# Kernel optimization log

Measured on AMD Instinct MI355X. Metric: run time of the kernel, lower is better.

## Reference

```python
import jax, jax.numpy as jnp
import numpy as np

D_MODEL = 512
NUM_HEADS = 8
D_K = D_MODEL // NUM_HEADS  # 64
LN_EPS = 1e-5


def setup_inputs() -> dict:
    key = jax.random.key(0)
    ks = jax.random.split(key, 6)
    B, S, D = 8, 1024, D_MODEL
    scale = 1.0 / np.sqrt(D)
    return {
        "query": jax.random.normal(ks[0], (B, S, D), jnp.float32),
        "key": jax.random.normal(ks[1], (B, S, D), jnp.float32),
        "value": jax.random.normal(ks[2], (B, S, D), jnp.float32),
        "Wq": jax.random.normal(ks[3], (D, D), jnp.float32) * scale,
        "bq": jnp.zeros((D,), jnp.float32),
        "Wk": jax.random.normal(ks[4], (D, D), jnp.float32) * scale,
        "bk": jnp.zeros((D,), jnp.float32),
        "Wo": jax.random.normal(ks[5], (D, D * NUM_HEADS), jnp.float32) * (1.0 / np.sqrt(D * NUM_HEADS)),
        "bo": jnp.zeros((D,), jnp.float32),
        "gamma": jnp.ones((D,), jnp.float32),
        "beta": jnp.zeros((D,), jnp.float32),
    }


def reference(query, key, value, Wq, bq, Wk, bk, Wo, bo, gamma, beta):
    B, S, D = value.shape
    h, dk = NUM_HEADS, D_K
    # QK projections -> [B, h, S, dk]
    q = (query @ Wq.T + bq).reshape(B, S, h, dk).transpose(0, 2, 1, 3)
    k = (key @ Wk.T + bk).reshape(B, S, h, dk).transpose(0, 2, 1, 3)
    # scaled dot-product scores [B, h, Sq, Sk]
    scores = jnp.einsum("bhqd,bhkd->bhqk", q, k) / jnp.sqrt(jnp.asarray(dk, q.dtype))
    attn = jax.nn.softmax(scores, axis=-1)
    # value broadcast across heads: value is [B, Sk, D] -> per-head output [B, h, Sq, D]
    x = jnp.einsum("bhqk,bkd->bhqd", attn, value)
    # concat heads -> [B, Sq, h*D], output projection back to D
    x = x.transpose(0, 2, 1, 3).reshape(B, S, h * D)
    x = x @ Wo.T + bo
    # residual + LayerNorm (dropout = identity in eval)
    y = value + x
    mu = jnp.mean(y, axis=-1, keepdims=True)
    var = jnp.var(y, axis=-1, keepdims=True)
    out = (y - mu) * jax.lax.rsqrt(var + LN_EPS) * gamma + beta
    return out, attn
```

## Files before the change

### kernel.cpp

```cpp
#include <hip/hip_runtime.h>
#include <hip/hip_bf16.h>

#define B_ 8
#define S_ 1024
#define D_ 512
#define H_ 8
#define DK_ 64
#define HD_ 4096

typedef __attribute__((ext_vector_type(8))) short bf16x8;
typedef __attribute__((ext_vector_type(4))) float f32x4;

static __device__ __forceinline__ unsigned short f2bf(float f) {
    unsigned u = __float_as_uint(f);
    unsigned r = (u + 0x7fffu + ((u >> 16) & 1u)) >> 16;
    return (unsigned short)r;
}

static __device__ __forceinline__ void gload16(const unsigned short* g, unsigned short* l) {
    __builtin_amdgcn_global_load_lds(
        (const __attribute__((address_space(1))) void*)g,
        (__attribute__((address_space(3))) void*)l, 16, 0, 0);
}

static __device__ __forceinline__ int plidx(int ql, int k) {
    return ql * 1024 + ((((k >> 3) ^ (ql & 7))) << 3) + (k & 7);
}

__global__ __launch_bounds__(256) void prep_kernel(
    const float* __restrict__ query, unsigned short* __restrict__ Xq,
    const float* __restrict__ key,   unsigned short* __restrict__ Xk,
    const float* __restrict__ Wq,    unsigned short* __restrict__ Wqbf,
    const float* __restrict__ Wk,    unsigned short* __restrict__ Wkbf,
    const float* __restrict__ Wo,    unsigned short* __restrict__ Wobf,
    const float* __restrict__ V,     unsigned short* __restrict__ Vt)
{
    __shared__ float tile[32][33];
    const int bid = blockIdx.x;
    const int t = threadIdx.x;
    if (bid < 10752) {
        const float* s; unsigned short* d; int lb;
        if      (bid < 4096) { s = query; d = Xq;   lb = bid; }
        else if (bid < 8192) { s = key;   d = Xk;   lb = bid - 4096; }
        else if (bid < 8448) { s = Wq;    d = Wqbf; lb = bid - 8192; }
        else if (bid < 8704) { s = Wk;    d = Wkbf; lb = bid - 8448; }
        else                 { s = Wo;    d = Wobf; lb = bid - 8704; }
        const size_t i = ((size_t)lb * 256 + t) * 4;
        float4 v = *(const float4*)&s[i];
        ushort4 u = { f2bf(v.x), f2bf(v.y), f2bf(v.z), f2bf(v.w) };
        *(ushort4*)&d[i] = u;
    } else {
        const int idx = bid - 10752;
        const int s0 = (idx & 31) * 32;
        const int e0 = ((idx >> 5) & 15) * 32;
        const int b  = idx >> 9;
        const int r = t >> 3, c4 = (t & 7) * 4;
        float4 v = *(const float4*)&V[((size_t)b * S_ + s0 + r) * D_ + e0 + c4];
        tile[r][c4 + 0] = v.x; tile[r][c4 + 1] = v.y;
        tile[r][c4 + 2] = v.z; tile[r][c4 + 3] = v.w;
        __syncthreads();
        ushort4 u;
        u.x = f2bf(tile[c4 + 0][r]); u.y = f2bf(tile[c4 + 1][r]);
        u.z = f2bf(tile[c4 + 2][r]); u.w = f2bf(tile[c4 + 3][r]);
        *(ushort4*)&Vt[((size_t)b * D_ + e0 + r) * S_ + s0 + c4] = u;
    }
}

template<int KDIM, int MT, int TN, int MODE>
static __device__ __forceinline__ void gemm_body(
    const unsigned short* __restrict__ A, const unsigned short* __restrict__ Bw,
    const float* __restrict__ bias, const float* __restrict__ Vres,
    void* __restrict__ Out, float scale, int nb)
{
    constexpr int NB = 512 / TN;
    constexpr int CF = TN / 32;
    constexpr int MR = MT / 32;
    const int m0 = (nb / NB) * MT;
    const int n0 = (nb % NB) * TN;

    __shared__ __align__(16) unsigned short As[2][MT * 32];
    __shared__ __align__(16) unsigned short Bs[2][TN * 32];

    const int t = threadIdx.x;
    const int wave = t >> 6, lane = t & 63;
    const int wr = wave >> 1, wc = wave & 1;
    const int lr = lane & 15, g = lane >> 4;
    const int gx = (g ^ (lr & 3)) << 3;

    f32x4 acc[MR][CF];
    #pragma unroll
    for (int r = 0; r < MR; ++r)
        #pragma unroll
        for (int c = 0; c < CF; ++c) acc[r][c] = (f32x4){0.f, 0.f, 0.f, 0.f};

    const int sub = lane >> 2;
    const int cb  = (((lane & 3) ^ (sub & 3)) << 3);

    auto stage = [&](int buf, int k0) {
        #pragma unroll
        for (int s = 0; s < MT / 64; ++s) {
            const int chunk = s * 4 + wave;
            const int row = chunk * 16 + sub;
            if constexpr (MODE == 0) {
                gload16(&A[(size_t)(m0 + row) * KDIM + k0 + cb], &As[buf][chunk * 512]);
            } else {
                const int m = m0 + row;
                const int bb = m >> 10, ss = m & 1023;
                const int h = k0 >> 9;
                gload16(&A[(((size_t)(bb * H_ + h)) * S_ + ss) * D_ + (k0 & 511) + cb],
                        &As[buf][chunk * 512]);
            }
        }
        #pragma unroll
        for (int s = 0; s < TN / 64; ++s) {
            const int chunk = s * 4 + wave;
            const int row = chunk * 16 + sub;
            gload16(&Bw[(size_t)(n0 + row) * KDIM + k0 + cb], &Bs[buf][chunk * 512]);
        }
    };
    auto compute = [&](int cur) {
        bf16x8 af[MR], bfr[CF];
        #pragma unroll
        for (int r = 0; r < MR; ++r)
            af[r] = *(const bf16x8*)&As[cur][(wr * (MT / 2) + r * 16 + lr) * 32 + gx];
        #pragma unroll
        for (int c = 0; c < CF; ++c)
            bfr[c] = *(const bf16x8*)&Bs[cur][(wc * (TN / 2) + c * 16 + lr) * 32 + gx];
        __builtin_amdgcn_s_setprio(1);
        #pragma unroll
        for (int c = 0; c < CF; ++c)
            #pragma unroll
            for (int r = 0; r < MR; ++r)
                acc[r][c] = __builtin_amdgcn_mfma_f32_16x16x32_bf16(af[r], bfr[c], acc[r][c], 0, 0, 0);
        __builtin_amdgcn_s_setprio(0);
    };

    const int NT = KDIM / 32;
    stage(0, 0);
    __syncthreads();
    int cur = 0;
    for (int tt = 0; tt < NT - 1; ++tt) {
        stage(cur ^ 1, (tt + 1) * 32);
        compute(cur);
        __syncthreads();
        cur ^= 1;
    }
    compute(cur);

    float bn[CF];
    #pragma unroll
    for (int c = 0; c < CF; ++c) bn[c] = bias[n0 + wc * (TN / 2) + c * 16 + lr];

    #pragma unroll
    for (int r = 0; r < MR; ++r) {
        #pragma unroll
        for (int c = 0; c < CF; ++c) {
            const int n = n0 + wc * (TN / 2) + c * 16 + lr;
            #pragma unroll
            for (int i = 0; i < 4; ++i) {
                const int m = m0 + wr * (MT / 2) + r * 16 + g * 4 + i;
                if constexpr (MODE == 0) {
                    const int srow = m & 1023, bb = m >> 10;
                    const int h = n >> 6, dk = n & 63;
                    ((unsigned short*)Out)[(((size_t)(bb * H_ + h)) * S_ + srow) * DK_ + dk] =
                        f2bf((acc[r][c][i] + bn[c]) * scale);
                } else {
                    const size_t oo = (size_t)m * D_ + n;
                    ((float*)Out)[oo] = acc[r][c][i] + bn[c] + Vres[oo];
                }
            }
        }
    }
}

__global__ __launch_bounds__(256) void proj2_kernel(
    const unsigned short* __restrict__ Xq, const unsigned short* __restrict__ Wqbf,
    const float* __restrict__ bq, unsigned short* __restrict__ Qbf,
    const unsigned short* __restrict__ Xk, const unsigned short* __restrict__ Wkbf,
    const float* __restrict__ bk, unsigned short* __restrict__ Kbf)
{
    const int o = blockIdx.x;
    const bool isQ = o < 512;
    const int ol = isQ ? o : o - 512;
    const int nb = (ol % 8) * 64 + ol / 8;
    gemm_body<512, 128, 64, 0>(isQ ? Xq : Xk, isQ ? Wqbf : Wkbf,
                               isQ ? bq : bk, nullptr,
                               (void*)(isQ ? Qbf : Kbf), isQ ? 0.125f : 1.0f, nb);
}

__global__ __launch_bounds__(256) void out_gemm(
    const unsigned short* __restrict__ AV, const unsigned short* __restrict__ Wobf,
    const float* __restrict__ bo, const float* __restrict__ Vres,
    float* __restrict__ Y)
{
    const int o = blockIdx.x;
    const int nb = (o % 8) * 64 + o / 8;
    gemm_body<4096, 64, 128, 1>(AV, Wobf, bo, Vres, (void*)Y, 0.f, nb);
}

__global__ __launch_bounds__(1024, 4) void fused_attn(
    const unsigned short* __restrict__ Qbf,
    const unsigned short* __restrict__ Kbf,
    const unsigned short* __restrict__ Vt,
    float* __restrict__ attn,
    unsigned short* __restrict__ AV)
{
    const int o = blockIdx.x;
    const int nb = (o & 7) * 128 + (o >> 3);
    const int bh = nb >> 4;
    const int q0 = (nb & 15) * 64;
    const int b = bh >> 3;
    const unsigned short* Qb = Qbf + (size_t)bh * S_ * DK_;
    const unsigned short* Kb = Kbf + (size_t)bh * S_ * DK_;
    const unsigned short* Vb = Vt + (size_t)b * D_ * S_;
    float* outp = attn + ((size_t)bh << 20);

    __shared__ unsigned short PL[64 * 1024];
    __shared__ float redm[64][16];
    __shared__ float rowm[64];

    const int t = threadIdx.x;
    const int wave = t >> 6, lane = t & 63;
    const int wcol = wave * 64;
    const int lr = lane & 15;
    const int g  = lane >> 4;

    f32x4 acc[4][4];
    #pragma unroll
    for (int r = 0; r < 4; ++r)
        #pragma unroll
        for (int c = 0; c < 4; ++c) acc[r][c] = (f32x4){0.f, 0.f, 0.f, 0.f};

    #pragma unroll
    for (int kk = 0; kk < 2; ++kk) {
        bf16x8 af[4];
        #pragma unroll
        for (int r = 0; r < 4; ++r)
            af[r] = *(const bf16x8*)&Kb[(size_t)(wcol + r * 16 + lr) * DK_ + kk * 32 + g * 8];
        bf16x8 qf[4];
        #pragma unroll
        for (int c = 0; c < 4; ++c)
            qf[c] = *(const bf16x8*)&Qb[(size_t)(q0 + c * 16 + lr) * DK_ + kk * 32 + g * 8];
        __builtin_amdgcn_s_setprio(1);
        #pragma unroll
        for (int r = 0; r < 4; ++r)
            #pragma unroll
            for (int c = 0; c < 4; ++c)
                acc[r][c] = __builtin_amdgcn_mfma_f32_16x16x32_bf16(af[r], qf[c], acc[r][c], 0, 0, 0);
        __builtin_amdgcn_s_setprio(0);
    }

    float sloc[4];
    #pragma unroll
    for (int c = 0; c < 4; ++c) {
        float s = 0.f;
        #pragma unroll
        for (int r = 0; r < 4; ++r)
            #pragma unroll
            for (int i = 0; i < 4; ++i) {
                float p = __expf(acc[r][c][i]);
                acc[r][c][i] = p;
                s += p;
            }
        s += __shfl_xor(s, 16);
        s += __shfl_xor(s, 32);
        sloc[c] = s;
    }
    if (lane < 16) {
        #pragma unroll
        for (int c = 0; c < 4; ++c) redm[c * 16 + lane][wave] = sloc[c];
    }
    __syncthreads();
    if (t < 64) {
        float s = redm[t][0];
        #pragma unroll
        for (int w = 1; w < 16; ++w) s += redm[t][w];
        rowm[t] = 1.0f / s;
    }
    __syncthreads();

    #pragma unroll
    for (int c = 0; c < 4; ++c) {
        const int ql = c * 16 + lr;
        const float ri = rowm[ql];
        float* rowp = outp + ((size_t)(q0 + ql) << 10);
        #pragma unroll
        for (int r = 0; r < 4; ++r) {
            f32x4 v = acc[r][c];
            v[0] *= ri; v[1] *= ri; v[2] *= ri; v[3] *= ri;
            const int k = wcol + r * 16 + g * 4;
            *(f32x4*)&rowp[k] = v;
            unsigned p01, p23;
            asm("v_cvt_pk_bf16_f32 %0, %1, %2" : "=v"(p01) : "v"(v[0]), "v"(v[1]));
            asm("v_cvt_pk_bf16_f32 %0, %1, %2" : "=v"(p23) : "v"(v[2]), "v"(v[3]));
            uint2 pk = { p01, p23 };
            *(uint2*)&PL[plidx(ql, k)] = pk;
        }
    }
    __syncthreads();

    const int we = wave * 32;
    f32x4 accv[4][2];
    #pragma unroll
    for (int r = 0; r < 4; ++r)
        #pragma unroll
        for (int c = 0; c < 2; ++c) accv[r][c] = (f32x4){0.f, 0.f, 0.f, 0.f};

    const unsigned short* vp0 = Vb + (size_t)(we + lr) * S_ + g * 8;
    const unsigned short* vp1 = Vb + (size_t)(we + 16 + lr) * S_ + g * 8;
    bf16x8 vf0 = *(const bf16x8*)vp0;
    bf16x8 vf1 = *(const bf16x8*)vp1;

    for (int k0 = 0; k0 < S_; k0 += 32) {
        const int kn = k0 + 32;
        bf16x8 nv0, nv1;
        if (kn < S_) {
            nv0 = *(const bf16x8*)(vp0 + kn);
            nv1 = *(const bf16x8*)(vp1 + kn);
        }
        bf16x8 pa[4];
        #pragma unroll
        for (int r = 0; r < 4; ++r)
            pa[r] = *(const bf16x8*)&PL[plidx(r * 16 + lr, k0 + g * 8)];
        __builtin_amdgcn_s_setprio(1);
        #pragma unroll
        for (int r = 0; r < 4; ++r)
            accv[r][0] = __builtin_amdgcn_mfma_f32_16x16x32_bf16(pa[r], vf0, accv[r][0], 0, 0, 0);
        #pragma unroll
        for (int r = 0; r < 4; ++r)
            accv[r][1] = __builtin_amdgcn_mfma_f32_16x16x32_bf16(pa[r], vf1, accv[r][1], 0, 0, 0);
        __builtin_amdgcn_s_setprio(0);
        if (kn < S_) { vf0 = nv0; vf1 = nv1; }
    }

    #pragma unroll
    for (int r = 0; r < 4; ++r) {
        #pragma unroll
        for (int c = 0; c < 2; ++c) {
            const int e = we + c * 16 + lr;
            #pragma unroll
            for (int i = 0; i < 4; ++i) {
                const int row = q0 + r * 16 + g * 4 + i;
                AV[((size_t)bh * S_ + row) * D_ + e] = f2bf(accv[r][c][i]);
            }
        }
    }
}

__global__ __launch_bounds__(256) void ln_kernel(
    float* __restrict__ Y, const float* __restrict__ gamma,
    const float* __restrict__ beta)
{
    const int lane = threadIdx.x & 63;
    const int wave = threadIdx.x >> 6;
    const size_t row = (size_t)blockIdx.x * 4 + wave;
    float* p = Y + row * D_;
    float4 v0 = *(float4*)&p[lane * 4];
    float4 v1 = *(float4*)&p[256 + lane * 4];
    float s = v0.x + v0.y + v0.z + v0.w + v1.x + v1.y + v1.z + v1.w;
    float q = v0.x * v0.x + v0.y * v0.y + v0.z * v0.z + v0.w * v0.w +
              v1.x * v1.x + v1.y * v1.y + v1.z * v1.z + v1.w * v1.w;
    #pragma unroll
    for (int m = 1; m < 64; m <<= 1) {
        s += __shfl_xor(s, m);
        q += __shfl_xor(q, m);
    }
    const float mu  = s * (1.f / 512.f);
    const float var = q * (1.f / 512.f) - mu * mu;
    const float r = rsqrtf(var + 1e-5f);
    const float4 g0 = *(const float4*)&gamma[lane * 4];
    const float4 g1 = *(const float4*)&gamma[256 + lane * 4];
    const float4 b0 = *(const float4*)&beta[lane * 4];
    const float4 b1 = *(const float4*)&beta[256 + lane * 4];
    v0.x = (v0.x - mu) * r * g0.x + b0.x;
    v0.y = (v0.y - mu) * r * g0.y + b0.y;
    v0.z = (v0.z - mu) * r * g0.z + b0.z;
    v0.w = (v0.w - mu) * r * g0.w + b0.w;
    v1.x = (v1.x - mu) * r * g1.x + b1.x;
    v1.y = (v1.y - mu) * r * g1.y + b1.y;
    v1.z = (v1.z - mu) * r * g1.z + b1.z;
    v1.w = (v1.w - mu) * r * g1.w + b1.w;
    *(float4*)&p[lane * 4] = v0;
    *(float4*)&p[256 + lane * 4] = v1;
}

extern "C" void kernel_launch(void* const* d_in, const int* in_sizes, int n_in,
                              void* d_out, int out_size, void* d_ws, size_t ws_size,
                              hipStream_t stream)
{
    const float* query = (const float*)d_in[0];
    const float* key   = (const float*)d_in[1];
    const float* value = (const float*)d_in[2];
    const float* Wq    = (const float*)d_in[3];
    const float* bq    = (const float*)d_in[4];
    const float* Wk    = (const float*)d_in[5];
    const float* bk    = (const float*)d_in[6];
    const float* Wo    = (const float*)d_in[7];
    const float* bo    = (const float*)d_in[8];
    const float* gamma = (const float*)d_in[9];
    const float* beta  = (const float*)d_in[10];

    float* out  = (float*)d_out;
    float* attn = out + (size_t)B_ * S_ * D_;
    char*  attnB = (char*)attn;

    char* ws = (char*)d_ws;
    unsigned short* AV   = (unsigned short*)ws;
    unsigned short* Vt   = (unsigned short*)(ws + ((size_t)64 << 20));
    unsigned short* Wobf = (unsigned short*)(ws + ((size_t)72 << 20));
    unsigned short* Qbf  = (unsigned short*)d_out;
    unsigned short* Kbf  = (unsigned short*)d_out + ((size_t)4 << 20);
    unsigned short* Xq   = (unsigned short*)(attnB + ((size_t)200 << 20));
    unsigned short* Xk   = (unsigned short*)(attnB + ((size_t)210 << 20));
    unsigned short* Wqbf = (unsigned short*)(attnB + ((size_t)220 << 20));
    unsigned short* Wkbf = (unsigned short*)(attnB + ((size_t)221 << 20));

    prep_kernel<<<14848, 256, 0, stream>>>(query, Xq, key, Xk, Wq, Wqbf,
                                           Wk, Wkbf, Wo, Wobf, value, Vt);
    proj2_kernel<<<1024, 256, 0, stream>>>(Xq, Wqbf, bq, Qbf, Xk, Wkbf, bk, Kbf);
    fused_attn<<<1024, 1024, 0, stream>>>(Qbf, Kbf, Vt, attn, AV);
    out_gemm<<<512, 256, 0, stream>>>(AV, Wobf, bo, value, out);
    ln_kernel<<<2048, 256, 0, stream>>>(out, gamma, beta);
}
```

Before: 333.1 us.

## Fuse output projection, residual and LayerNorm into one full-row GEMM kernel

Replaces the separate output GEMM and LayerNorm kernels with one kernel where each block computes a 32x512 full-row tile. Residual add, row statistics via shuffles and LDS, and normalization happen in the epilogue. This removes an extra round trip of the 16 MB output and a launch. In exchange, each block streams all of Wo from cache, raising total weight traffic, and runs with only 256 blocks of 4 waves.

```diff
diff --git a/kernel.cpp b/kernel.cpp
--- a/kernel.cpp
+++ b/kernel.cpp
@@ -66,10 +66,10 @@
     }
 }
 
-template<int KDIM, int MT, int TN, int MODE>
+template<int KDIM, int MT, int TN>
 static __device__ __forceinline__ void gemm_body(
     const unsigned short* __restrict__ A, const unsigned short* __restrict__ Bw,
-    const float* __restrict__ bias, const float* __restrict__ Vres,
+    const float* __restrict__ bias,
     void* __restrict__ Out, float scale, int nb)
 {
     constexpr int NB = 512 / TN;
@@ -101,15 +101,7 @@
         for (int s = 0; s < MT / 64; ++s) {
             const int chunk = s * 4 + wave;
             const int row = chunk * 16 + sub;
-            if constexpr (MODE == 0) {
-                gload16(&A[(size_t)(m0 + row) * KDIM + k0 + cb], &As[buf][chunk * 512]);
-            } else {
-                const int m = m0 + row;
-                const int bb = m >> 10, ss = m & 1023;
-                const int h = k0 >> 9;
-                gload16(&A[(((size_t)(bb * H_ + h)) * S_ + ss) * D_ + (k0 & 511) + cb],
-                        &As[buf][chunk * 512]);
-            }
+            gload16(&A[(size_t)(m0 + row) * KDIM + k0 + cb], &As[buf][chunk * 512]);
         }
         #pragma unroll
         for (int s = 0; s < TN / 64; ++s) {
@@ -159,15 +151,10 @@
             #pragma unroll
             for (int i = 0; i < 4; ++i) {
                 const int m = m0 + wr * (MT / 2) + r * 16 + g * 4 + i;
-                if constexpr (MODE == 0) {
-                    const int srow = m & 1023, bb = m >> 10;
-                    const int h = n >> 6, dk = n & 63;
-                    ((unsigned short*)Out)[(((size_t)(bb * H_ + h)) * S_ + srow) * DK_ + dk] =
-                        f2bf((acc[r][c][i] + bn[c]) * scale);
-                } else {
-                    const size_t oo = (size_t)m * D_ + n;
-                    ((float*)Out)[oo] = acc[r][c][i] + bn[c] + Vres[oo];
-                }
+                const int srow = m & 1023, bb = m >> 10;
+                const int h = n >> 6, dk = n & 63;
+                ((unsigned short*)Out)[(((size_t)(bb * H_ + h)) * S_ + srow) * DK_ + dk] =
+                    f2bf((acc[r][c][i] + bn[c]) * scale);
             }
         }
     }
@@ -183,19 +170,130 @@
     const bool isQ = o < 512;
     const int ol = isQ ? o : o - 512;
     const int nb = (ol % 8) * 64 + ol / 8;
-    gemm_body<512, 128, 64, 0>(isQ ? Xq : Xk, isQ ? Wqbf : Wkbf,
-                               isQ ? bq : bk, nullptr,
-                               (void*)(isQ ? Qbf : Kbf), isQ ? 0.125f : 1.0f, nb);
-}
-
-__global__ __launch_bounds__(256) void out_gemm(
-    const unsigned short* __restrict__ AV, const unsigned short* __restrict__ Wobf,
+    gemm_body<512, 128, 64>(isQ ? Xq : Xk, isQ ? Wqbf : Wkbf,
+                            isQ ? bq : bk,
+                            (void*)(isQ ? Qbf : Kbf), isQ ? 0.125f : 1.0f, nb);
+}
+
+__global__ __launch_bounds__(256) void out_ln_gemm(
+    const unsigned short* __restrict__ AV,
+    const unsigned short* __restrict__ Wobf,
     const float* __restrict__ bo, const float* __restrict__ Vres,
+    const float* __restrict__ gamma, const float* __restrict__ beta,
     float* __restrict__ Y)
 {
     const int o = blockIdx.x;
-    const int nb = (o % 8) * 64 + o / 8;
-    gemm_body<4096, 64, 128, 1>(AV, Wobf, bo, Vres, (void*)Y, 0.f, nb);
+    const int nb = (o % 8) * 32 + o / 8;
+    const int m0 = nb * 32;
+
+    __shared__ __align__(16) unsigned short As[2][32 * 32];
+    __shared__ __align__(16) unsigned short Bs[2][512 * 32];
+    __shared__ float lsum[32][4], lsq[32][4];
+
+    const int t = threadIdx.x;
+    const int wave = t >> 6, lane = t & 63;
+    const int lr = lane & 15, g = lane >> 4;
+    const int gx = (g ^ (lr & 3)) << 3;
+    const int sub = lane >> 2;
+    const int cb  = (((lane & 3) ^ (sub & 3)) << 3);
+
+    f32x4 acc[2][8];
+    #pragma unroll
+    for (int r = 0; r < 2; ++r)
+        #pragma unroll
+        for (int c = 0; c < 8; ++c) acc[r][c] = (f32x4){0.f, 0.f, 0.f, 0.f};
+
+    auto stage = [&](int buf, int k0) {
+        if (wave < 2) {
+            const int row = wave * 16 + sub;
+            const int m = m0 + row;
+            const int bb = m >> 10, ss = m & 1023;
+            const int h = k0 >> 9;
+            gload16(&AV[(((size_t)(bb * H_ + h)) * S_ + ss) * D_ + (k0 & 511) + cb],
+                    &As[buf][wave * 512]);
+        }
+        #pragma unroll
+        for (int s = 0; s < 8; ++s) {
+            const int chunk = s * 4 + wave;
+            const int row = chunk * 16 + sub;
+            gload16(&Wobf[(size_t)row * HD_ + k0 + cb], &Bs[buf][chunk * 512]);
+        }
+    };
+    auto compute = [&](int cur) {
+        bf16x8 af[2], bfr[8];
+        #pragma unroll
+        for (int r = 0; r < 2; ++r)
+            af[r] = *(const bf16x8*)&As[cur][(r * 16 + lr) * 32 + gx];
+        #pragma unroll
+        for (int c = 0; c < 8; ++c)
+            bfr[c] = *(const bf16x8*)&Bs[cur][(wave * 128 + c * 16 + lr) * 32 + gx];
+        __builtin_amdgcn_s_setprio(1);
+        #pragma unroll
+        for (int c = 0; c < 8; ++c)
+            #pragma unroll
+            for (int r = 0; r < 2; ++r)
+                acc[r][c] = __builtin_amdgcn_mfma_f32_16x16x32_bf16(af[r], bfr[c], acc[r][c], 0, 0, 0);
+        __builtin_amdgcn_s_setprio(0);
+    };
+
+    stage(0, 0);
+    __syncthreads();
+    int cur = 0;
+    for (int tt = 0; tt < 127; ++tt) {
+        stage(cur ^ 1, (tt + 1) * 32);
+        compute(cur);
+        __syncthreads();
+        cur ^= 1;
+    }
+    compute(cur);
+
+    float bn[8], gm[8], bt[8];
+    #pragma unroll
+    for (int c = 0; c < 8; ++c) {
+        const int n = wave * 128 + c * 16 + lr;
+        bn[c] = bo[n]; gm[c] = gamma[n]; bt[c] = beta[n];
+    }
+    #pragma unroll
+    for (int r = 0; r < 2; ++r) {
+        #pragma unroll
+        for (int i = 0; i < 4; ++i) {
+            const int row = r * 16 + g * 4 + i;
+            const int mrow = m0 + row;
+            float s = 0.f, q = 0.f;
+            #pragma unroll
+            for (int c = 0; c < 8; ++c) {
+                const int n = wave * 128 + c * 16 + lr;
+                float y = acc[r][c][i] + bn[c] + Vres[(size_t)mrow * D_ + n];
+                acc[r][c][i] = y;
+                s += y; q += y * y;
+            }
+            #pragma unroll
+            for (int m = 1; m < 16; m <<= 1) {
+                s += __shfl_xor(s, m);
+                q += __shfl_xor(q, m);
+            }
+            if (lr == 0) { lsum[row][wave] = s; lsq[row][wave] = q; }
+        }
+    }
+    __syncthreads();
+    #pragma unroll
+    for (int r = 0; r < 2; ++r) {
+        #pragma unroll
+        for (int i = 0; i < 4; ++i) {
+            const int row = r * 16 + g * 4 + i;
+            const int mrow = m0 + row;
+            const float st = lsum[row][0] + lsum[row][1] + lsum[row][2] + lsum[row][3];
+            const float qt = lsq[row][0] + lsq[row][1] + lsq[row][2] + lsq[row][3];
+            const float mu = st * (1.f / 512.f);
+            const float var = qt * (1.f / 512.f) - mu * mu;
+            const float rs = rsqrtf(var + 1e-5f);
+            #pragma unroll
+            for (int c = 0; c < 8; ++c) {
+                const int n = wave * 128 + c * 16 + lr;
+                Y[(size_t)mrow * D_ + n] = (acc[r][c][i] - mu) * rs * gm[c] + bt[c];
+            }
+        }
+    }
 }
 
 __global__ __launch_bounds__(1024, 4) void fused_attn(
@@ -345,43 +443,6 @@
             }
         }
     }
-}
-
-__global__ __launch_bounds__(256) void ln_kernel(
-    float* __restrict__ Y, const float* __restrict__ gamma,
-    const float* __restrict__ beta)
-{
-    const int lane = threadIdx.x & 63;
-    const int wave = threadIdx.x >> 6;
-    const size_t row = (size_t)blockIdx.x * 4 + wave;
-    float* p = Y + row * D_;
-    float4 v0 = *(float4*)&p[lane * 4];
-    float4 v1 = *(float4*)&p[256 + lane * 4];
-    float s = v0.x + v0.y + v0.z + v0.w + v1.x + v1.y + v1.z + v1.w;
-    float q = v0.x * v0.x + v0.y * v0.y + v0.z * v0.z + v0.w * v0.w +
-              v1.x * v1.x + v1.y * v1.y + v1.z * v1.z + v1.w * v1.w;
-    #pragma unroll
-    for (int m = 1; m < 64; m <<= 1) {
-        s += __shfl_xor(s, m);
-        q += __shfl_xor(q, m);
-    }
-    const float mu  = s * (1.f / 512.f);
-    const float var = q * (1.f / 512.f) - mu * mu;
-    const float r = rsqrtf(var + 1e-5f);
-    const float4 g0 = *(const float4*)&gamma[lane * 4];
-    const float4 g1 = *(const float4*)&gamma[256 + lane * 4];
-    const float4 b0 = *(const float4*)&beta[lane * 4];
-    const float4 b1 = *(const float4*)&beta[256 + lane * 4];
-    v0.x = (v0.x - mu) * r * g0.x + b0.x;
-    v0.y = (v0.y - mu) * r * g0.y + b0.y;
-    v0.z = (v0.z - mu) * r * g0.z + b0.z;
-    v0.w = (v0.w - mu) * r * g0.w + b0.w;
-    v1.x = (v1.x - mu) * r * g1.x + b1.x;
-    v1.y = (v1.y - mu) * r * g1.y + b1.y;
-    v1.z = (v1.z - mu) * r * g1.z + b1.z;
-    v1.w = (v1.w - mu) * r * g1.w + b1.w;
-    *(float4*)&p[lane * 4] = v0;
-    *(float4*)&p[256 + lane * 4] = v1;
 }
 
 extern "C" void kernel_launch(void* const* d_in, const int* in_sizes, int n_in,
@@ -419,6 +480,5 @@
                                            Wk, Wkbf, Wo, Wobf, value, Vt);
     proj2_kernel<<<1024, 256, 0, stream>>>(Xq, Wqbf, bq, Qbf, Xk, Wkbf, bk, Kbf);
     fused_attn<<<1024, 1024, 0, stream>>>(Qbf, Kbf, Vt, attn, AV);
-    out_gemm<<<512, 256, 0, stream>>>(AV, Wobf, bo, value, out);
-    ln_kernel<<<2048, 256, 0, stream>>>(out, gamma, beta);
-}
+    out_ln_gemm<<<256, 256, 0, stream>>>(AV, Wobf, bo, value, gamma, beta, out);
+}
```

Result: slower. 408.2 us (+22.5%).
